# Performance work log

Measured on AMD Instinct MI355X. Metric: run time of the kernel, lower is better.

The kernel has to match this reference:

```python
import jax, jax.numpy as jnp
import numpy as np

N_NODES = 100000
N_EDGES = 1600000
F_IN = 256
HID = 256
N_CLS = 40


def _glorot(key, shape):
    lim = float(np.sqrt(6.0 / (shape[0] + shape[1])))
    return jax.random.uniform(key, shape, jnp.float32, -lim, lim)


def setup_inputs() -> dict:
    key = jax.random.key(0)
    ks = jax.random.split(key, 8)
    x = jax.random.normal(ks[0], (N_NODES, F_IN), jnp.float32)
    edge_index = jax.random.randint(ks[1], (2, N_EDGES), 0, N_NODES, jnp.int64)
    return {
        "x": x,
        "edge_index": edge_index,
        "W1": _glorot(ks[2], (F_IN, HID)),
        "b1": jnp.zeros((HID,), jnp.float32),
        "W2": _glorot(ks[3], (HID, HID)),
        "b2": jnp.zeros((HID,), jnp.float32),
        "W3": _glorot(ks[4], (HID, N_CLS)),
        "b3": jnp.zeros((N_CLS,), jnp.float32),
    }


def _gcn_conv(x, W, b, src, dst, norm, num_nodes):
    # linear transform first (PyG GCNConv), then normalized scatter-add
    h = x @ W                                   # [N, out]
    msg = h[src] * norm[:, None]                # [E+N, out] gathered messages
    out = jax.ops.segment_sum(msg, dst, num_segments=num_nodes)
    return out + b


def reference(x, edge_index, W1, b1, W2, b2, W3, b3):
    n = x.shape[0]
    loop = jnp.arange(n, dtype=edge_index.dtype)
    src = jnp.concatenate([edge_index[0], loop])  # add self-loops
    dst = jnp.concatenate([edge_index[1], loop])
    # symmetric GCN normalization: deg^{-1/2}[src] * deg^{-1/2}[dst]
    deg = jax.ops.segment_sum(jnp.ones_like(dst, dtype=x.dtype), dst, num_segments=n)
    dinv = jnp.where(deg > 0, jax.lax.rsqrt(deg), 0.0)
    norm = dinv[src] * dinv[dst]

    h = jax.nn.relu(_gcn_conv(x, W1, b1, src, dst, norm, n))  # dropout p=0.0 is identity
    h = jax.nn.relu(_gcn_conv(h, W2, b2, src, dst, norm, n))
    out = _gcn_conv(h, W3, b3, src, dst, norm, n)             # logits [N, num_classes]
    return out
```

## Files before the change

kernel.cpp:

```cpp
#include <hip/hip_runtime.h>
#include <hip/hip_bf16.h>
#include <cstdint>
#include <cstddef>

#define NNODES 100000
#define NEDGES 1600000
#define NCLS 40
#define NBLK_SCAN 391
#define NBUCK 391
#define BCAP 5120
#define NBLKB 256
#define CHUNK 6250
#define MPAD 100096

typedef _Float16 f16;
typedef _Float16 f16x8 __attribute__((ext_vector_type(8)));
typedef float f32x4 __attribute__((ext_vector_type(4)));

__device__ inline float h2f(unsigned short u) {
    f16 h; __builtin_memcpy(&h, &u, 2); return (float)h;
}
__device__ inline unsigned short f2h(float f) {
    f16 h = (f16)f; unsigned short u; __builtin_memcpy(&u, &h, 2); return u;
}
__device__ inline void gload_lds16(const void* g, void* l) {
    __builtin_amdgcn_global_load_lds((const __attribute__((address_space(1))) unsigned int*)g,
                                     (__attribute__((address_space(3))) unsigned int*)l, 16, 0, 0);
}
__device__ inline void acc8(float* a, uint4 v) {
    a[0] += h2f((unsigned short)(v.x & 0xffff)); a[1] += h2f((unsigned short)(v.x >> 16));
    a[2] += h2f((unsigned short)(v.y & 0xffff)); a[3] += h2f((unsigned short)(v.y >> 16));
    a[4] += h2f((unsigned short)(v.z & 0xffff)); a[5] += h2f((unsigned short)(v.z >> 16));
    a[6] += h2f((unsigned short)(v.w & 0xffff)); a[7] += h2f((unsigned short)(v.w >> 16));
}

__global__ void k_detect(const int* __restrict__ ei, int* __restrict__ flag) {
    if (threadIdx.x == 0 && blockIdx.x == 0) {
        int nz = 0;
        for (int i = 1; i < 256; i += 2) nz |= ei[i];
        *flag = (nz == 0) ? 1 : 0;
    }
}

__global__ __launch_bounds__(256) void k_bucket(const int* __restrict__ ei,
        const int* __restrict__ flag, int* __restrict__ gbcnt, int2* __restrict__ bedge) {
    __shared__ int lcnt[NBUCK], lbase[NBUCK], lcur[NBUCK];
    const int t = threadIdx.x;
    const int is64 = *flag;
    for (int i = t; i < NBUCK; i += 256) lcnt[i] = 0;
    __syncthreads();
    const int e0 = blockIdx.x * CHUNK;
    for (int i = t; i < CHUNK; i += 256) {
        int e = e0 + i;
        int d = is64 ? ei[2 * ((size_t)NEDGES + e)] : ei[NEDGES + e];
        atomicAdd(&lcnt[d >> 8], 1);
    }
    __syncthreads();
    for (int i = t; i < NBUCK; i += 256) {
        int c = lcnt[i];
        lbase[i] = c ? atomicAdd(&gbcnt[i], c) : 0;
        lcur[i] = 0;
    }
    __syncthreads();
    for (int i = t; i < CHUNK; i += 256) {
        int e = e0 + i;
        int s, d;
        if (is64) { s = ei[2 * (size_t)e]; d = ei[2 * ((size_t)NEDGES + e)]; }
        else      { s = ei[e];             d = ei[NEDGES + e]; }
        int b = d >> 8;
        int p = lbase[b] + atomicAdd(&lcur[b], 1);
        if (p < BCAP) bedge[(size_t)b * BCAP + p] = make_int2(s, d);
    }
}

__global__ __launch_bounds__(256) void k_cnt(const int* __restrict__ gbcnt,
        const int2* __restrict__ bedge, int* __restrict__ cnt) {
    __shared__ int lc[256];
    const int t = threadIdx.x, b = blockIdx.x;
    lc[t] = 0;
    __syncthreads();
    const int ne = min(gbcnt[b], BCAP);
    const int2* be = bedge + (size_t)b * BCAP;
    for (int i = t; i < ne; i += 256)
        atomicAdd(&lc[be[i].y & 255], 1);
    __syncthreads();
    int node = b * 256 + t;
    if (node < NNODES) cnt[node] = lc[t];
}

__global__ __launch_bounds__(256) void k_dinv(const int* __restrict__ cnt, float* __restrict__ dinv) {
    int i = blockIdx.x * 256 + threadIdx.x;
    if (i < MPAD) dinv[i] = (i < NNODES) ? rsqrtf((float)(cnt[i] + 1)) : 0.f;
}

__global__ __launch_bounds__(256) void k_scan1(const int* __restrict__ cnt,
        int* __restrict__ incl, int* __restrict__ blksum) {
    __shared__ int sm[256];
    const int t = threadIdx.x;
    int i = blockIdx.x * 256 + t;
    int v = (i < NNODES) ? (cnt[i] + 1) : 0;
    sm[t] = v;
    __syncthreads();
    for (int d = 1; d < 256; d <<= 1) {
        int x = (t >= d) ? sm[t - d] : 0;
        __syncthreads();
        sm[t] += x;
        __syncthreads();
    }
    if (i < NNODES) incl[i] = sm[t];
    if (t == 255) blksum[blockIdx.x] = sm[255];
}

__global__ __launch_bounds__(512) void k_scan2(const int* __restrict__ blksum, int* __restrict__ blkoff) {
    __shared__ int sm[512];
    const int t = threadIdx.x;
    int v = (t < NBLK_SCAN) ? blksum[t] : 0;
    sm[t] = v;
    __syncthreads();
    for (int d = 1; d < 512; d <<= 1) {
        int x = (t >= d) ? sm[t - d] : 0;
        __syncthreads();
        sm[t] += x;
        __syncthreads();
    }
    if (t < NBLK_SCAN) blkoff[t] = sm[t] - v;
}

__global__ __launch_bounds__(256) void k_scan3(const int* __restrict__ incl,
        const int* __restrict__ blkoff, int* __restrict__ offs) {
    int i = blockIdx.x * 256 + threadIdx.x;
    if (i < NNODES) offs[i + 1] = incl[i] + blkoff[blockIdx.x];
    if (i == 0) offs[0] = 0;
}

__global__ __launch_bounds__(256) void k_self(const int* __restrict__ offs, int* __restrict__ esrc) {
    int i = blockIdx.x * 256 + threadIdx.x;
    if (i < NNODES) esrc[offs[i]] = i;
}

__global__ __launch_bounds__(256) void k_fill2(const int* __restrict__ gbcnt,
        const int2* __restrict__ bedge, const int* __restrict__ offs, int* __restrict__ esrc) {
    __shared__ int loff[256], lcur[256];
    const int t = threadIdx.x, b = blockIdx.x;
    int node = b * 256 + t;
    loff[t] = (node < NNODES) ? offs[node] : 0;
    lcur[t] = 0;
    __syncthreads();
    const int ne = min(gbcnt[b], BCAP);
    const int2* be = bedge + (size_t)b * BCAP;
    for (int i = t; i < ne; i += 256) {
        int2 sd = be[i];
        int li = sd.y & 255;
        int p = loff[li] + 1 + atomicAdd(&lcur[li], 1);
        esrc[p] = sd.x;
    }
}

__global__ __launch_bounds__(256) void k_wt(const float* __restrict__ W, unsigned short* __restrict__ WT) {
    int k = blockIdx.x;
    int n = threadIdx.x;
    WT[n * 256 + k] = f2h(W[k * 256 + n]);
}

template<bool A32>
__global__ __launch_bounds__(256) void gemm_core(const void* __restrict__ Ap,
        const unsigned short* __restrict__ BT, unsigned short* __restrict__ C,
        const float* __restrict__ dinv) {
    __shared__ __align__(16) char lds[65536];
    const int t = threadIdx.x;
    const int w = t >> 6, l = t & 63;
    const int bm = blockIdx.x * 128;
    const int bn = blockIdx.y * 128;
    const int lr = l >> 3, ls = l & 7;
    const unsigned short* A16 = (const unsigned short*)Ap;
    const float* A32p = (const float*)Ap;

    auto stageB = [&](int buf, int k0) {
        char* base = lds + buf * 32768 + 16384;
#pragma unroll
        for (int i = 0; i < 4; ++i) {
            int r = w * 32 + i * 8 + lr;
            int sl = ls ^ (r & 7);
            const char* gB = (const char*)BT + (size_t)(bn + r) * 512 + (size_t)k0 * 2 + sl * 16;
            gload_lds16(gB, base + (w * 32 + i * 8) * 128);
        }
    };
    auto stageA16 = [&](int buf, int k0) {
        char* base = lds + buf * 32768;
#pragma unroll
        for (int i = 0; i < 4; ++i) {
            int r = w * 32 + i * 8 + lr;
            int sl = ls ^ (r & 7);
            const char* gA = (const char*)A16 + (size_t)(bm + r) * 512 + (size_t)k0 * 2 + sl * 16;
            gload_lds16(gA, base + (w * 32 + i * 8) * 128);
        }
    };
    float4 areg[8];
    auto issueA32 = [&](int k0) {
#pragma unroll
        for (int i = 0; i < 8; ++i) {
            int tt = i * 256 + t;
            int r = tt >> 4, q = tt & 15;
            float4 v = make_float4(0.f, 0.f, 0.f, 0.f);
            if (bm + r < NNODES) v = *(const float4*)(A32p + (size_t)(bm + r) * 256 + k0 + q * 4);
            areg[i] = v;
        }
    };
    auto writeA32 = [&](int buf) {
        char* base = lds + buf * 32768;
#pragma unroll
        for (int i = 0; i < 8; ++i) {
            int tt = i * 256 + t;
            int r = tt >> 4, q = tt & 15;
            f16 h4[4] = {(f16)areg[i].x, (f16)areg[i].y, (f16)areg[i].z, (f16)areg[i].w};
            char* dst = base + r * 128 + (((q >> 1) ^ (r & 7)) * 16) + (q & 1) * 8;
            __builtin_memcpy(dst, h4, 8);
        }
    };

    f32x4 acc[4][4];
#pragma unroll
    for (int m = 0; m < 4; ++m)
#pragma unroll
        for (int n = 0; n < 4; ++n)
            acc[m][n] = (f32x4){0.f, 0.f, 0.f, 0.f};

    const int frow = l & 15, fk = l >> 4;
    const int r0w = (w >> 1) * 64, c0w = (w & 1) * 64;

    if constexpr (A32) { issueA32(0); } else { stageA16(0, 0); }
    stageB(0, 0);
    if constexpr (A32) { writeA32(0); }
    __syncthreads();
    for (int kt = 0; kt < 4; ++kt) {
        const int buf = kt & 1;
        if (kt < 3) {
            if constexpr (A32) { issueA32((kt + 1) * 64); } else { stageA16(buf ^ 1, (kt + 1) * 64); }
            stageB(buf ^ 1, (kt + 1) * 64);
        }
        const char* As = lds + buf * 32768;
        const char* Bs = As + 16384;
#pragma unroll
        for (int ks = 0; ks < 2; ++ks) {
            f16x8 af[4], bf[4];
#pragma unroll
            for (int m = 0; m < 4; ++m) {
                int ra = r0w + m * 16 + frow;
                af[m] = *(const f16x8*)(As + ra * 128 + (((ks * 4 + fk) ^ (ra & 7)) * 16));
            }
#pragma unroll
            for (int n = 0; n < 4; ++n) {
                int rb = c0w + n * 16 + frow;
                bf[n] = *(const f16x8*)(Bs + rb * 128 + (((ks * 4 + fk) ^ (rb & 7)) * 16));
            }
#pragma unroll
            for (int m = 0; m < 4; ++m)
#pragma unroll
                for (int n = 0; n < 4; ++n)
                    acc[m][n] = __builtin_amdgcn_mfma_f32_16x16x32_f16(af[m], bf[n], acc[m][n], 0, 0, 0);
        }
        if constexpr (A32) { if (kt < 3) writeA32(buf ^ 1); }
        __syncthreads();
    }

    unsigned short* Cs = (unsigned short*)lds;
    const int crow = (l >> 4) * 4, ccol = l & 15;
#pragma unroll
    for (int m = 0; m < 4; ++m) {
        float4 dv = *(const float4*)(dinv + bm + r0w + m * 16 + crow);
        float d4[4] = {dv.x, dv.y, dv.z, dv.w};
#pragma unroll
        for (int n = 0; n < 4; ++n)
#pragma unroll
            for (int r = 0; r < 4; ++r)
                Cs[(r0w + m * 16 + crow + r) * 136 + c0w + n * 16 + ccol] = f2h(acc[m][n][r] * d4[r]);
    }
    __syncthreads();
#pragma unroll
    for (int i = 0; i < 8; ++i) {
        int row = i * 16 + (t >> 4);
        int cs = t & 15;
        uint4 v = *(const uint4*)(Cs + row * 136 + cs * 8);
        *(uint4*)((char*)C + (size_t)(bm + row) * 512 + bn * 2 + cs * 16) = v;
    }
}

__global__ __launch_bounds__(256) void gemm40_h16(const unsigned short* __restrict__ A,
        const float* __restrict__ B, unsigned short* __restrict__ C, int M,
        const float* __restrict__ dinv) {
    __shared__ float As[16][68];
    __shared__ float Bs[16][44];
    const int t  = threadIdx.x;
    const int bm = blockIdx.x * 64;
    const int tx = t & 7;
    const int ty = t >> 3;
    const int ar = t >> 2, ac = (t & 3) << 2;
    float acc[2][5] = {};
    for (int k0 = 0; k0 < 256; k0 += 16) {
        float4 av = make_float4(0, 0, 0, 0);
        int r0 = bm + ar;
        if (r0 < M) {
            ushort4 ah = *(const ushort4*)(A + (size_t)r0 * 256 + k0 + ac);
            av = make_float4(h2f(ah.x), h2f(ah.y), h2f(ah.z), h2f(ah.w));
        }
        float4 bv = make_float4(0, 0, 0, 0);
        int brow = t / 10, bcol = (t % 10) * 4;
        if (t < 160) bv = *(const float4*)(B + (size_t)(k0 + brow) * 40 + bcol);
        __syncthreads();
        As[ac + 0][ar] = av.x; As[ac + 1][ar] = av.y; As[ac + 2][ar] = av.z; As[ac + 3][ar] = av.w;
        if (t < 160) {
            Bs[brow][bcol] = bv.x; Bs[brow][bcol + 1] = bv.y;
            Bs[brow][bcol + 2] = bv.z; Bs[brow][bcol + 3] = bv.w;
        }
        __syncthreads();
#pragma unroll
        for (int kk = 0; kk < 16; ++kk) {
            float a0 = As[kk][ty * 2], a1 = As[kk][ty * 2 + 1];
            float b[5];
#pragma unroll
            for (int j = 0; j < 5; ++j) b[j] = Bs[kk][tx * 5 + j];
#pragma unroll
            for (int j = 0; j < 5; ++j) {
                acc[0][j] = fmaf(a0, b[j], acc[0][j]);
                acc[1][j] = fmaf(a1, b[j], acc[1][j]);
            }
        }
    }
#pragma unroll
    for (int i = 0; i < 2; ++i) {
        int row = bm + ty * 2 + i;
        if (row < M) {
            float dv = dinv[row];
#pragma unroll
            for (int j = 0; j < 5; ++j) C[(size_t)row * 40 + tx * 5 + j] = f2h(acc[i][j] * dv);
        }
    }
}

__global__ __launch_bounds__(256) void agg_v2(const unsigned short* __restrict__ T,
        const int* __restrict__ esrc, const int* __restrict__ offs,
        const float* __restrict__ dinv, const float* __restrict__ bias,
        unsigned short* __restrict__ outh) {
    int node = blockIdx.x * 4 + (threadIdx.x >> 6);
    if (node >= NNODES) return;
    const int l = threadIdx.x & 63;
    const int half = l >> 5, sub = l & 31;
    const uint4* Tv = (const uint4*)T;
    float a[8] = {0.f, 0.f, 0.f, 0.f, 0.f, 0.f, 0.f, 0.f};
    const int e0 = offs[node], e1 = offs[node + 1];
    int e = e0 + half;
    for (; e + 6 < e1; e += 8) {
        int s0 = esrc[e], s1 = esrc[e + 2], s2 = esrc[e + 4], s3 = esrc[e + 6];
        uint4 u0 = Tv[(size_t)s0 * 32 + sub];
        uint4 u1 = Tv[(size_t)s1 * 32 + sub];
        uint4 u2 = Tv[(size_t)s2 * 32 + sub];
        uint4 u3 = Tv[(size_t)s3 * 32 + sub];
        acc8(a, u0); acc8(a, u1); acc8(a, u2); acc8(a, u3);
    }
    for (; e < e1; e += 2) {
        int s0 = esrc[e];
        uint4 u0 = Tv[(size_t)s0 * 32 + sub];
        acc8(a, u0);
    }
#pragma unroll
    for (int j = 0; j < 8; ++j) a[j] += __shfl_xor(a[j], 32, 64);
    if (!half) {
        float di = dinv[node];
        float4 b0 = *(const float4*)(bias + sub * 8);
        float4 b1 = *(const float4*)(bias + sub * 8 + 4);
        float r0 = fmaxf(fmaf(a[0], di, b0.x), 0.f);
        float r1 = fmaxf(fmaf(a[1], di, b0.y), 0.f);
        float r2 = fmaxf(fmaf(a[2], di, b0.z), 0.f);
        float r3 = fmaxf(fmaf(a[3], di, b0.w), 0.f);
        float r4 = fmaxf(fmaf(a[4], di, b1.x), 0.f);
        float r5 = fmaxf(fmaf(a[5], di, b1.y), 0.f);
        float r6 = fmaxf(fmaf(a[6], di, b1.z), 0.f);
        float r7 = fmaxf(fmaf(a[7], di, b1.w), 0.f);
        uint4 o;
        o.x = (unsigned)f2h(r0) | ((unsigned)f2h(r1) << 16);
        o.y = (unsigned)f2h(r2) | ((unsigned)f2h(r3) << 16);
        o.z = (unsigned)f2h(r4) | ((unsigned)f2h(r5) << 16);
        o.w = (unsigned)f2h(r6) | ((unsigned)f2h(r7) << 16);
        ((uint4*)outh)[(size_t)node * 32 + sub] = o;
    }
}

__global__ __launch_bounds__(256) void agg_out_v2(const unsigned short* __restrict__ T,
        const int* __restrict__ esrc, const int* __restrict__ offs,
        const float* __restrict__ dinv, const float* __restrict__ bias,
        float* __restrict__ out) {
    int node = blockIdx.x * 4 + (threadIdx.x >> 6);
    if (node >= NNODES) return;
    const int l = threadIdx.x & 63;
    const int g = l >> 4, sl = l & 15;
    const bool act = sl < 10;
    float a0 = 0.f, a1 = 0.f, a2 = 0.f, a3 = 0.f;
    const int e0 = offs[node], e1 = offs[node + 1];
    for (int e = e0 + g; e < e1; e += 4) {
        int s = esrc[e];
        if (act) {
            ushort4 u = *(const ushort4*)(T + (size_t)s * 40 + sl * 4);
            a0 += h2f(u.x); a1 += h2f(u.y); a2 += h2f(u.z); a3 += h2f(u.w);
        }
    }
    a0 += __shfl_xor(a0, 16, 64); a1 += __shfl_xor(a1, 16, 64);
    a2 += __shfl_xor(a2, 16, 64); a3 += __shfl_xor(a3, 16, 64);
    a0 += __shfl_xor(a0, 32, 64); a1 += __shfl_xor(a1, 32, 64);
    a2 += __shfl_xor(a2, 32, 64); a3 += __shfl_xor(a3, 32, 64);
    if (g == 0 && act) {
        float di = dinv[node];
        float4 bv = *(const float4*)(bias + sl * 4);
        float4 o = make_float4(fmaf(a0, di, bv.x), fmaf(a1, di, bv.y),
                               fmaf(a2, di, bv.z), fmaf(a3, di, bv.w));
        *(float4*)(out + (size_t)node * 40 + sl * 4) = o;
    }
}

extern "C" void kernel_launch(void* const* d_in, const int* in_sizes, int n_in,
                              void* d_out, int out_size, void* d_ws, size_t ws_size,
                              hipStream_t stream) {
    const float* x  = (const float*)d_in[0];
    const int*   ei = (const int*)d_in[1];
    const float* W1 = (const float*)d_in[2];
    const float* b1 = (const float*)d_in[3];
    const float* W2 = (const float*)d_in[4];
    const float* b2 = (const float*)d_in[5];
    const float* W3 = (const float*)d_in[6];
    const float* b3 = (const float*)d_in[7];
    float* out = (float*)d_out;

    char* ws = (char*)d_ws;
    size_t o = 0;
    unsigned short* tbA  = (unsigned short*)(ws + o); o += (size_t)MPAD * 256 * 2;
    unsigned short* tbB  = (unsigned short*)(ws + o); o += (size_t)MPAD * 256 * 2;
    unsigned short* tb40 = (unsigned short*)(ws + o); o += (size_t)NNODES * NCLS * 2;
    unsigned short* W1T  = (unsigned short*)(ws + o); o += 131072;
    unsigned short* W2T  = (unsigned short*)(ws + o); o += 131072;
    int2* bedge  = (int2*)(ws + o);  o += (size_t)NBUCK * BCAP * 8;
    int* gbcnt   = (int*)(ws + o);   o += 2048;
    int* esrc    = (int*)(ws + o);   o += (size_t)(NEDGES + NNODES) * 4;
    int* cnt     = (int*)(ws + o);   o += 400128;
    int* offs    = (int*)(ws + o);   o += 400384;
    float* dinv  = (float*)(ws + o); o += 400384;
    int* incl    = (int*)(ws + o);   o += 400128;
    int* blksum  = (int*)(ws + o);   o += 2048;
    int* blkoff  = (int*)(ws + o);   o += 2048;
    int* flag    = (int*)(ws + o);   o += 256;
    if (ws_size < o) return;

    hipMemsetAsync(gbcnt, 0, 2048, stream);
    hipMemsetAsync(tbB + (size_t)NNODES * 256, 0, (MPAD - NNODES) * 512, stream);

    k_detect<<<1, 64, 0, stream>>>(ei, flag);
    k_bucket<<<NBLKB, 256, 0, stream>>>(ei, flag, gbcnt, bedge);
    k_cnt<<<NBUCK, 256, 0, stream>>>(gbcnt, bedge, cnt);
    k_dinv<<<(MPAD + 255) / 256, 256, 0, stream>>>(cnt, dinv);
    k_scan1<<<NBLK_SCAN, 256, 0, stream>>>(cnt, incl, blksum);
    k_scan2<<<1, 512, 0, stream>>>(blksum, blkoff);
    k_scan3<<<NBLK_SCAN, 256, 0, stream>>>(incl, blkoff, offs);
    k_self<<<NBLK_SCAN, 256, 0, stream>>>(offs, esrc);
    k_fill2<<<NBUCK, 256, 0, stream>>>(gbcnt, bedge, offs, esrc);

    k_wt<<<256, 256, 0, stream>>>(W1, W1T);
    k_wt<<<256, 256, 0, stream>>>(W2, W2T);

    dim3 gg(MPAD / 128, 2), b256(256);
    gemm_core<true><<<gg, b256, 0, stream>>>(x, W1T, tbA, dinv);
    agg_v2<<<NNODES / 4, 256, 0, stream>>>(tbA, esrc, offs, dinv, b1, tbB);
    gemm_core<false><<<gg, b256, 0, stream>>>(tbB, W2T, tbA, dinv);
    agg_v2<<<NNODES / 4, 256, 0, stream>>>(tbA, esrc, offs, dinv, b2, tbB);
    gemm40_h16<<<(NNODES + 63) / 64, 256, 0, stream>>>(tbB, W3, tb40, NNODES, dinv);
    agg_out_v2<<<NNODES / 4, 256, 0, stream>>>(tb40, esrc, offs, dinv, b3, out);
}
```

Baseline: 545.0 us.

## Use MFMA GEMM for final layer and wave-level index broadcast in aggregation

Replaces the scalar FP32 40-column GEMM with the MFMA gemm_core path, using a zero-padded transposed W3 and a narrow output store. The aggregation kernels now load up to 64 edge indices per wave at once and broadcast them with readlane/shfl, so each lane covers 4 features instead of splitting edges across half-waves. Accumulation uses v_fma_mix_f32 to fuse the fp16-to-fp32 conversion with the add. The final GEMM does wasted work on padded columns, and the aggregation now issues one 8-byte load per lane instead of 16-byte loads.

```diff
diff --git a/kernel.cpp b/kernel.cpp
--- a/kernel.cpp
+++ b/kernel.cpp
@@ -27,11 +27,11 @@
     __builtin_amdgcn_global_load_lds((const __attribute__((address_space(1))) unsigned int*)g,
                                      (__attribute__((address_space(3))) unsigned int*)l, 16, 0, 0);
 }
-__device__ inline void acc8(float* a, uint4 v) {
-    a[0] += h2f((unsigned short)(v.x & 0xffff)); a[1] += h2f((unsigned short)(v.x >> 16));
-    a[2] += h2f((unsigned short)(v.y & 0xffff)); a[3] += h2f((unsigned short)(v.y >> 16));
-    a[4] += h2f((unsigned short)(v.z & 0xffff)); a[5] += h2f((unsigned short)(v.z >> 16));
-    a[6] += h2f((unsigned short)(v.w & 0xffff)); a[7] += h2f((unsigned short)(v.w >> 16));
+__device__ inline void fmix2(float& alo, float& ahi, unsigned u, float one) {
+    asm("v_fma_mix_f32 %0, %1, %2, %0 op_sel:[0,0,0] op_sel_hi:[1,0,0]"
+        : "+v"(alo) : "v"(u), "v"(one));
+    asm("v_fma_mix_f32 %0, %1, %2, %0 op_sel:[1,0,0] op_sel_hi:[1,0,0]"
+        : "+v"(ahi) : "v"(u), "v"(one));
 }
 
 __global__ void k_detect(const int* __restrict__ ei, int* __restrict__ flag) {
@@ -162,7 +162,13 @@
     WT[n * 256 + k] = f2h(W[k * 256 + n]);
 }
 
-template<bool A32>
+__global__ __launch_bounds__(256) void k_wt3(const float* __restrict__ W, unsigned short* __restrict__ WT) {
+    int n = blockIdx.x;
+    int k = threadIdx.x;
+    WT[n * 256 + k] = (n < NCLS) ? f2h(W[k * NCLS + n]) : (unsigned short)0;
+}
+
+template<bool A32, bool NARROW>
 __global__ __launch_bounds__(256) void gemm_core(const void* __restrict__ Ap,
         const unsigned short* __restrict__ BT, unsigned short* __restrict__ C,
         const float* __restrict__ dinv) {
@@ -281,111 +287,68 @@
         int row = i * 16 + (t >> 4);
         int cs = t & 15;
         uint4 v = *(const uint4*)(Cs + row * 136 + cs * 8);
-        *(uint4*)((char*)C + (size_t)(bm + row) * 512 + bn * 2 + cs * 16) = v;
-    }
-}
-
-__global__ __launch_bounds__(256) void gemm40_h16(const unsigned short* __restrict__ A,
-        const float* __restrict__ B, unsigned short* __restrict__ C, int M,
-        const float* __restrict__ dinv) {
-    __shared__ float As[16][68];
-    __shared__ float Bs[16][44];
-    const int t  = threadIdx.x;
-    const int bm = blockIdx.x * 64;
-    const int tx = t & 7;
-    const int ty = t >> 3;
-    const int ar = t >> 2, ac = (t & 3) << 2;
-    float acc[2][5] = {};
-    for (int k0 = 0; k0 < 256; k0 += 16) {
-        float4 av = make_float4(0, 0, 0, 0);
-        int r0 = bm + ar;
-        if (r0 < M) {
-            ushort4 ah = *(const ushort4*)(A + (size_t)r0 * 256 + k0 + ac);
-            av = make_float4(h2f(ah.x), h2f(ah.y), h2f(ah.z), h2f(ah.w));
-        }
-        float4 bv = make_float4(0, 0, 0, 0);
-        int brow = t / 10, bcol = (t % 10) * 4;
-        if (t < 160) bv = *(const float4*)(B + (size_t)(k0 + brow) * 40 + bcol);
-        __syncthreads();
-        As[ac + 0][ar] = av.x; As[ac + 1][ar] = av.y; As[ac + 2][ar] = av.z; As[ac + 3][ar] = av.w;
-        if (t < 160) {
-            Bs[brow][bcol] = bv.x; Bs[brow][bcol + 1] = bv.y;
-            Bs[brow][bcol + 2] = bv.z; Bs[brow][bcol + 3] = bv.w;
-        }
-        __syncthreads();
-#pragma unroll
-        for (int kk = 0; kk < 16; ++kk) {
-            float a0 = As[kk][ty * 2], a1 = As[kk][ty * 2 + 1];
-            float b[5];
-#pragma unroll
-            for (int j = 0; j < 5; ++j) b[j] = Bs[kk][tx * 5 + j];
-#pragma unroll
-            for (int j = 0; j < 5; ++j) {
-                acc[0][j] = fmaf(a0, b[j], acc[0][j]);
-                acc[1][j] = fmaf(a1, b[j], acc[1][j]);
-            }
-        }
-    }
-#pragma unroll
-    for (int i = 0; i < 2; ++i) {
-        int row = bm + ty * 2 + i;
-        if (row < M) {
-            float dv = dinv[row];
-#pragma unroll
-            for (int j = 0; j < 5; ++j) C[(size_t)row * 40 + tx * 5 + j] = f2h(acc[i][j] * dv);
-        }
-    }
-}
-
-__global__ __launch_bounds__(256) void agg_v2(const unsigned short* __restrict__ T,
+        if constexpr (NARROW) {
+            if (cs < 5)
+                *(uint4*)((char*)C + (size_t)(bm + row) * 80 + cs * 16) = v;
+        } else {
+            *(uint4*)((char*)C + (size_t)(bm + row) * 512 + bn * 2 + cs * 16) = v;
+        }
+    }
+}
+
+__global__ __launch_bounds__(256) void agg_v3(const unsigned short* __restrict__ T,
         const int* __restrict__ esrc, const int* __restrict__ offs,
         const float* __restrict__ dinv, const float* __restrict__ bias,
         unsigned short* __restrict__ outh) {
     int node = blockIdx.x * 4 + (threadIdx.x >> 6);
     if (node >= NNODES) return;
     const int l = threadIdx.x & 63;
-    const int half = l >> 5, sub = l & 31;
-    const uint4* Tv = (const uint4*)T;
-    float a[8] = {0.f, 0.f, 0.f, 0.f, 0.f, 0.f, 0.f, 0.f};
+    const float one = 1.0f;
     const int e0 = offs[node], e1 = offs[node + 1];
-    int e = e0 + half;
-    for (; e + 6 < e1; e += 8) {
-        int s0 = esrc[e], s1 = esrc[e + 2], s2 = esrc[e + 4], s3 = esrc[e + 6];
-        uint4 u0 = Tv[(size_t)s0 * 32 + sub];
-        uint4 u1 = Tv[(size_t)s1 * 32 + sub];
-        uint4 u2 = Tv[(size_t)s2 * 32 + sub];
-        uint4 u3 = Tv[(size_t)s3 * 32 + sub];
-        acc8(a, u0); acc8(a, u1); acc8(a, u2); acc8(a, u3);
-    }
-    for (; e < e1; e += 2) {
-        int s0 = esrc[e];
-        uint4 u0 = Tv[(size_t)s0 * 32 + sub];
-        acc8(a, u0);
-    }
-#pragma unroll
-    for (int j = 0; j < 8; ++j) a[j] += __shfl_xor(a[j], 32, 64);
-    if (!half) {
-        float di = dinv[node];
-        float4 b0 = *(const float4*)(bias + sub * 8);
-        float4 b1 = *(const float4*)(bias + sub * 8 + 4);
-        float r0 = fmaxf(fmaf(a[0], di, b0.x), 0.f);
-        float r1 = fmaxf(fmaf(a[1], di, b0.y), 0.f);
-        float r2 = fmaxf(fmaf(a[2], di, b0.z), 0.f);
-        float r3 = fmaxf(fmaf(a[3], di, b0.w), 0.f);
-        float r4 = fmaxf(fmaf(a[4], di, b1.x), 0.f);
-        float r5 = fmaxf(fmaf(a[5], di, b1.y), 0.f);
-        float r6 = fmaxf(fmaf(a[6], di, b1.z), 0.f);
-        float r7 = fmaxf(fmaf(a[7], di, b1.w), 0.f);
-        uint4 o;
-        o.x = (unsigned)f2h(r0) | ((unsigned)f2h(r1) << 16);
-        o.y = (unsigned)f2h(r2) | ((unsigned)f2h(r3) << 16);
-        o.z = (unsigned)f2h(r4) | ((unsigned)f2h(r5) << 16);
-        o.w = (unsigned)f2h(r6) | ((unsigned)f2h(r7) << 16);
-        ((uint4*)outh)[(size_t)node * 32 + sub] = o;
-    }
-}
-
-__global__ __launch_bounds__(256) void agg_out_v2(const unsigned short* __restrict__ T,
+    const int ne = e1 - e0;
+    const int myidx = esrc[e0 + min(l, ne - 1)];
+    const char* Tb = (const char*)T;
+    float a0 = 0.f, a1 = 0.f, a2 = 0.f, a3 = 0.f;
+    const int nreg = min(ne, 64);
+    int j = 0;
+    for (; j + 8 <= nreg; j += 8) {
+        uint2 u[8];
+#pragma unroll
+        for (int q = 0; q < 8; ++q) {
+            int s = __builtin_amdgcn_readlane(myidx, j + q);
+            u[q] = *(const uint2*)(Tb + (size_t)s * 512 + l * 8);
+        }
+#pragma unroll
+        for (int q = 0; q < 8; ++q) {
+            fmix2(a0, a1, u[q].x, one);
+            fmix2(a2, a3, u[q].y, one);
+        }
+    }
+    for (; j < nreg; ++j) {
+        int s = __builtin_amdgcn_readlane(myidx, j);
+        uint2 u = *(const uint2*)(Tb + (size_t)s * 512 + l * 8);
+        fmix2(a0, a1, u.x, one);
+        fmix2(a2, a3, u.y, one);
+    }
+    for (int e = e0 + 64; e < e1; ++e) {
+        int s = esrc[e];
+        uint2 u = *(const uint2*)(Tb + (size_t)s * 512 + l * 8);
+        fmix2(a0, a1, u.x, one);
+        fmix2(a2, a3, u.y, one);
+    }
+    float di = dinv[node];
+    float4 bv = *(const float4*)(bias + l * 4);
+    float r0 = fmaxf(fmaf(a0, di, bv.x), 0.f);
+    float r1 = fmaxf(fmaf(a1, di, bv.y), 0.f);
+    float r2 = fmaxf(fmaf(a2, di, bv.z), 0.f);
+    float r3 = fmaxf(fmaf(a3, di, bv.w), 0.f);
+    uint2 o;
+    o.x = (unsigned)f2h(r0) | ((unsigned)f2h(r1) << 16);
+    o.y = (unsigned)f2h(r2) | ((unsigned)f2h(r3) << 16);
+    *(uint2*)(outh + (size_t)node * 256 + l * 4) = o;
+}
+
+__global__ __launch_bounds__(256) void agg_out_v3(const unsigned short* __restrict__ T,
         const int* __restrict__ esrc, const int* __restrict__ offs,
         const float* __restrict__ dinv, const float* __restrict__ bias,
         float* __restrict__ out) {
@@ -394,13 +357,28 @@
     const int l = threadIdx.x & 63;
     const int g = l >> 4, sl = l & 15;
     const bool act = sl < 10;
+    const float one = 1.0f;
+    const int e0 = offs[node], e1 = offs[node + 1];
+    const int ne = e1 - e0;
+    const int myidx = esrc[e0 + min(l, ne - 1)];
+    const int nreg = min(ne, 64);
+    const char* Tb = (const char*)T;
     float a0 = 0.f, a1 = 0.f, a2 = 0.f, a3 = 0.f;
-    const int e0 = offs[node], e1 = offs[node + 1];
-    for (int e = e0 + g; e < e1; e += 4) {
+    for (int j = 0; j < nreg; j += 4) {
+        int jj = j + g;
+        int s = __shfl(myidx, jj, 64);
+        if (jj < nreg && act) {
+            uint2 u = *(const uint2*)(Tb + (size_t)s * 80 + sl * 8);
+            fmix2(a0, a1, u.x, one);
+            fmix2(a2, a3, u.y, one);
+        }
+    }
+    for (int e = e0 + 64 + g; e < e1; e += 4) {
         int s = esrc[e];
         if (act) {
-            ushort4 u = *(const ushort4*)(T + (size_t)s * 40 + sl * 4);
-            a0 += h2f(u.x); a1 += h2f(u.y); a2 += h2f(u.z); a3 += h2f(u.w);
+            uint2 u = *(const uint2*)(Tb + (size_t)s * 80 + sl * 8);
+            fmix2(a0, a1, u.x, one);
+            fmix2(a2, a3, u.y, one);
         }
     }
     a0 += __shfl_xor(a0, 16, 64); a1 += __shfl_xor(a1, 16, 64);
@@ -433,9 +411,10 @@
     size_t o = 0;
     unsigned short* tbA  = (unsigned short*)(ws + o); o += (size_t)MPAD * 256 * 2;
     unsigned short* tbB  = (unsigned short*)(ws + o); o += (size_t)MPAD * 256 * 2;
-    unsigned short* tb40 = (unsigned short*)(ws + o); o += (size_t)NNODES * NCLS * 2;
+    unsigned short* tb40 = (unsigned short*)(ws + o); o += (size_t)MPAD * NCLS * 2;
     unsigned short* W1T  = (unsigned short*)(ws + o); o += 131072;
     unsigned short* W2T  = (unsigned short*)(ws + o); o += 131072;
+    unsigned short* W3T  = (unsigned short*)(ws + o); o += 65536;
     int2* bedge  = (int2*)(ws + o);  o += (size_t)NBUCK * BCAP * 8;
     int* gbcnt   = (int*)(ws + o);   o += 2048;
     int* esrc    = (int*)(ws + o);   o += (size_t)(NEDGES + NNODES) * 4;
@@ -463,12 +442,13 @@
 
     k_wt<<<256, 256, 0, stream>>>(W1, W1T);
     k_wt<<<256, 256, 0, stream>>>(W2, W2T);
+    k_wt3<<<128, 256, 0, stream>>>(W3, W3T);
 
     dim3 gg(MPAD / 128, 2), b256(256);
-    gemm_core<true><<<gg, b256, 0, stream>>>(x, W1T, tbA, dinv);
-    agg_v2<<<NNODES / 4, 256, 0, stream>>>(tbA, esrc, offs, dinv, b1, tbB);
-    gemm_core<false><<<gg, b256, 0, stream>>>(tbB, W2T, tbA, dinv);
-    agg_v2<<<NNODES / 4, 256, 0, stream>>>(tbA, esrc, offs, dinv, b2, tbB);
-    gemm40_h16<<<(NNODES + 63) / 64, 256, 0, stream>>>(tbB, W3, tb40, NNODES, dinv);
-    agg_out_v2<<<NNODES / 4, 256, 0, stream>>>(tb40, esrc, offs, dinv, b3, out);
-}
+    gemm_core<true, false><<<gg, b256, 0, stream>>>(x, W1T, tbA, dinv);
+    agg_v3<<<NNODES / 4, 256, 0, stream>>>(tbA, esrc, offs, dinv, b1, tbB);
+    gemm_core<false, false><<<gg, b256, 0, stream>>>(tbB, W2T, tbA, dinv);
+    agg_v3<<<NNODES / 4, 256, 0, stream>>>(tbA, esrc, offs, dinv, b2, tbB);
+    gemm_core<false, true><<<dim3(MPAD / 128, 1), b256, 0, stream>>>(tbB, W3T, tb40, dinv);
+    agg_out_v3<<<NNODES / 4, 256, 0, stream>>>(tb40, esrc, offs, dinv, b3, out);
+}
```

After: 492.2 us. 1.11x faster.
